# Optimization experiments

Hardware: AMD Instinct MI355X
Metric: run time of the kernel (lower is better)

Reference implementation:

```python
import jax, jax.numpy as jnp
import numpy as np

N = 10000
E = 320000
D = 256


def setup_inputs() -> dict:
    key = jax.random.key(0)
    ks = jax.random.split(key, 10)
    s = 1.0 / np.sqrt(D)
    return {
        "x0": jax.random.normal(ks[0], (N, D), jnp.float32),
        "edge_index": jax.random.randint(ks[1], (2, E), 0, N, jnp.int32),
        "W1": jax.random.normal(ks[2], (D, D), jnp.float32) * s,
        "b1": jax.random.normal(ks[3], (D,), jnp.float32) * s,
        "W2": jax.random.normal(ks[4], (D, D), jnp.float32) * s,
        "b2": jax.random.normal(ks[5], (D,), jnp.float32) * s,
        "wa1": jax.random.normal(ks[6], (D,), jnp.float32) * s,
        "ba1": jax.random.normal(ks[7], (1,), jnp.float32) * s,
        "wa2": jax.random.normal(ks[8], (D,), jnp.float32) * s,
        "ba2": jax.random.normal(ks[9], (1,), jnp.float32) * s,
    }


def reference(x0, edge_index, W1, b1, W2, b2, wa1, ba1, wa2, ba2):
    n = x0.shape[0]
    leaky = lambda v: jax.nn.leaky_relu(v, 0.2)
    x0_i = leaky(x0 @ W1 + b1)                      # [N, D]
    x0_j = leaky(x0 @ W2 + b2)                      # [N, D]
    a1 = x0_i @ wa1 + ba1[0]                        # [N]
    a2 = x0_j @ wa2 + ba2[0]                        # [N]
    row, col = edge_index[0], edge_index[1]
    # sigmoid(a_1 + a_2.T)[row, col] without the dense N x N intermediate
    att = jax.nn.sigmoid(a1[row] + a2[col])         # [E]
    msg = att[:, None] * x0_j[col]                  # [E, D]
    out = jax.ops.segment_sum(msg, row, num_segments=n)  # sparse.mm(attention, x0_j)
    return out + x0
```

## Files before the change

kernel.cpp:

```cpp
#include <hip/hip_runtime.h>
#include <math.h>

#define D 256
#define CAP 128
#define APAD 264

typedef float f32x4 __attribute__((ext_vector_type(4)));
typedef short s16x8 __attribute__((ext_vector_type(8)));
typedef unsigned short u16x8 __attribute__((ext_vector_type(8)));

static __device__ __forceinline__ unsigned short f2bf(float x) {
    union { float f; unsigned u; } v; v.f = x;
    unsigned r = v.u + 0x7fff + ((v.u >> 16) & 1);
    return (unsigned short)(r >> 16);
}
static __device__ __forceinline__ float bf2f(unsigned short h) {
    union { unsigned u; float f; } v; v.u = ((unsigned)h) << 16;
    return v.f;
}

__global__ __launch_bounds__(256) void k_init(
    const float* __restrict__ W1, const float* __restrict__ W2,
    unsigned short* __restrict__ wt, int* __restrict__ curp, int n)
{
    const int i = blockIdx.x * 256 + threadIdx.x;
    if (i < 2 * D * D) {
        int k = i >> 9;
        int j = i & 511;
        float v = (j < D) ? W1[(size_t)k * D + j] : W2[(size_t)k * D + (j - D)];
        wt[(size_t)j * D + k] = f2bf(v);
    }
    if (i < n * 32) curp[i] = 0;
}

__global__ __launch_bounds__(256) void k_mfma_rank(
    const float* __restrict__ x0, const unsigned short* __restrict__ wt,
    const float* __restrict__ b1, const float* __restrict__ b2,
    const float* __restrict__ wa1, const float* __restrict__ wa2,
    const float* __restrict__ ba1, const float* __restrict__ ba2,
    const int* __restrict__ rows, const int* __restrict__ cols,
    int* __restrict__ curp, int* __restrict__ perm,
    unsigned short* __restrict__ x0j, float* __restrict__ a1,
    float* __restrict__ a2, int n, int e, int nrb)
{
    __shared__ unsigned short Atile[32][APAD];
    __shared__ float part[4][32];
    const int t = threadIdx.x;

    if ((int)blockIdx.x < nrb) {
        const int i0 = (blockIdx.x * 256 + t) * 8;
        if (i0 + 7 < e) {
            int4 ra = *(const int4*)&rows[i0];
            int4 rb4 = *(const int4*)&rows[i0 + 4];
            int4 ca = *(const int4*)&cols[i0];
            int4 cb4 = *(const int4*)&cols[i0 + 4];
            int s0 = atomicAdd(&curp[(size_t)ra.x << 5], 1);
            int s1 = atomicAdd(&curp[(size_t)ra.y << 5], 1);
            int s2 = atomicAdd(&curp[(size_t)ra.z << 5], 1);
            int s3 = atomicAdd(&curp[(size_t)ra.w << 5], 1);
            int s4 = atomicAdd(&curp[(size_t)rb4.x << 5], 1);
            int s5 = atomicAdd(&curp[(size_t)rb4.y << 5], 1);
            int s6 = atomicAdd(&curp[(size_t)rb4.z << 5], 1);
            int s7 = atomicAdd(&curp[(size_t)rb4.w << 5], 1);
            if (s0 < CAP) perm[(size_t)ra.x * CAP + s0] = ca.x;
            if (s1 < CAP) perm[(size_t)ra.y * CAP + s1] = ca.y;
            if (s2 < CAP) perm[(size_t)ra.z * CAP + s2] = ca.z;
            if (s3 < CAP) perm[(size_t)ra.w * CAP + s3] = ca.w;
            if (s4 < CAP) perm[(size_t)rb4.x * CAP + s4] = cb4.x;
            if (s5 < CAP) perm[(size_t)rb4.y * CAP + s5] = cb4.y;
            if (s6 < CAP) perm[(size_t)rb4.z * CAP + s6] = cb4.z;
            if (s7 < CAP) perm[(size_t)rb4.w * CAP + s7] = cb4.w;
        } else {
            for (int i = i0; i < e; ++i) {
                int r = rows[i];
                int slot = atomicAdd(&curp[(size_t)r << 5], 1);
                if (slot < CAP) perm[(size_t)r * CAP + slot] = cols[i];
            }
        }
        return;
    }

    const int lane = t & 63, w = t >> 6;
    const int rb = (blockIdx.x - nrb) * 32;
    const int lr = lane & 15;
    const int kg = lane >> 4;

    for (int s = t; s < 32 * 32; s += 256) {
        const int row = s >> 5, seg = s & 31;
        int gr = rb + row; if (gr >= n) gr = n - 1;
        f32x4 v0 = *(const f32x4*)&x0[(size_t)gr * D + seg * 8];
        f32x4 v1 = *(const f32x4*)&x0[(size_t)gr * D + seg * 8 + 4];
        u16x8 o;
        o[0] = f2bf(v0.x); o[1] = f2bf(v0.y); o[2] = f2bf(v0.z); o[3] = f2bf(v0.w);
        o[4] = f2bf(v1.x); o[5] = f2bf(v1.y); o[6] = f2bf(v1.z); o[7] = f2bf(v1.w);
        *(u16x8*)&Atile[row][seg * 8] = o;
    }
    __syncthreads();

    const int cb = w * 128;
    f32x4 acc[2][8] = {};

    #pragma unroll
    for (int ks = 0; ks < 8; ++ks) {
        const int k0 = ks * 32 + kg * 8;
        s16x8 af[2];
        af[0] = *(const s16x8*)&Atile[lr][k0];
        af[1] = *(const s16x8*)&Atile[16 + lr][k0];
        s16x8 bfr[8];
        #pragma unroll
        for (int cf = 0; cf < 8; ++cf)
            bfr[cf] = *(const s16x8*)&wt[(size_t)(cb + cf * 16 + lr) * D + k0];
        #pragma unroll
        for (int rf = 0; rf < 2; ++rf)
            #pragma unroll
            for (int cf = 0; cf < 8; ++cf)
                acc[rf][cf] = __builtin_amdgcn_mfma_f32_16x16x32_bf16(
                    af[rf], bfr[cf], acc[rf][cf], 0, 0, 0);
    }

    const bool isW2 = (w >= 2);
    const float* wav  = isW2 ? wa2 : wa1;
    const float* bias = isW2 ? b2  : b1;
    const int crel = cb - (isW2 ? D : 0);

    float rs[2][4] = {};
    #pragma unroll
    for (int rf = 0; rf < 2; ++rf) {
        #pragma unroll
        for (int cf = 0; cf < 8; ++cf) {
            const int col = crel + cf * 16 + lr;
            const float bv = bias[col], wv = wav[col];
            #pragma unroll
            for (int r = 0; r < 4; ++r) {
                float v = acc[rf][cf][r] + bv;
                v = (v > 0.0f) ? v : 0.2f * v;
                const int row = rb + rf * 16 + kg * 4 + r;
                if (isW2 && row < n) x0j[(size_t)row * D + col] = f2bf(v);
                rs[rf][r] += v * wv;
            }
        }
    }

    #pragma unroll
    for (int rf = 0; rf < 2; ++rf)
        #pragma unroll
        for (int r = 0; r < 4; ++r) {
            float s = rs[rf][r];
            s += __shfl_xor(s, 1, 64);
            s += __shfl_xor(s, 2, 64);
            s += __shfl_xor(s, 4, 64);
            s += __shfl_xor(s, 8, 64);
            if (lr == 0) part[w][rf * 16 + kg * 4 + r] = s;
        }
    __syncthreads();
    if (t < 32) {
        const int row = rb + t;
        if (row < n) {
            a1[row] = part[0][t] + part[1][t] + ba1[0] + ba2[0];
            a2[row] = part[2][t] + part[3][t];
        }
    }
}

__global__ __launch_bounds__(256) void k_agg(
    const unsigned short* __restrict__ x0j, const float* __restrict__ x0,
    const float* __restrict__ a1, const float* __restrict__ a2,
    const int* __restrict__ curp, const int* __restrict__ perm,
    float* __restrict__ out, int n, int nbh)
{
    __shared__ int   scol[4][CAP + 4];
    __shared__ float satt[4][CAP + 4];

    const int w = threadIdx.x >> 6, lane = threadIdx.x & 63;
    const int q = lane >> 4, hl = lane & 15;
    const int phase = blockIdx.x / nbh;
    const int row = (blockIdx.x % nbh) * 4 + w;

    int deg = 0;
    if (row < n) {
        deg = curp[(size_t)row << 5];
        if (deg > CAP) deg = CAP;
        const size_t pbase = (size_t)row * CAP;
        const float a1r = a1[row];

        for (int i = lane; i < deg; i += 64) {
            int c = perm[pbase + i];
            scol[w][i] = c;
            satt[w][i] = 1.0f / (1.0f + __expf(-(a1r + a2[c])));
        }
        if (lane < 4) {
            scol[w][deg + lane] = 0;
            satt[w][deg + lane] = 0.0f;
        }
    }
    __syncthreads();
    if (row >= n) return;

    const int degp = (deg + 3) & ~3;
    const int cbase = phase * 128 + hl * 8;

    float acc[8];
    #pragma unroll
    for (int k = 0; k < 8; ++k) acc[k] = 0.0f;

    for (int j = 0; j < degp; j += 4) {
        const int idx = j + q;
        const float a = satt[w][idx];
        const int   c = scol[w][idx];
        u16x8 v = *(const u16x8*)&x0j[(size_t)c * D + cbase];
        #pragma unroll
        for (int k = 0; k < 8; ++k) acc[k] += a * bf2f(v[k]);
    }

    #pragma unroll
    for (int k = 0; k < 8; ++k) acc[k] += __shfl_xor(acc[k], 16, 64);
    #pragma unroll
    for (int k = 0; k < 8; ++k) acc[k] += __shfl_xor(acc[k], 32, 64);

    float s0, s1;
    if      (q == 0) { s0 = acc[0]; s1 = acc[1]; }
    else if (q == 1) { s0 = acc[2]; s1 = acc[3]; }
    else if (q == 2) { s0 = acc[4]; s1 = acc[5]; }
    else             { s0 = acc[6]; s1 = acc[7]; }

    const int col = cbase + q * 2;
    float2 r = *(const float2*)&x0[(size_t)row * D + col];
    float2 o;
    o.x = r.x + s0; o.y = r.y + s1;
    *(float2*)&out[(size_t)row * D + col] = o;
}

extern "C" void kernel_launch(void* const* d_in, const int* in_sizes, int n_in,
                              void* d_out, int out_size, void* d_ws, size_t ws_size,
                              hipStream_t stream)
{
    const float* x0  = (const float*)d_in[0];
    const int*   ei  = (const int*)d_in[1];
    const float* W1  = (const float*)d_in[2];
    const float* b1  = (const float*)d_in[3];
    const float* W2  = (const float*)d_in[4];
    const float* b2  = (const float*)d_in[5];
    const float* wa1 = (const float*)d_in[6];
    const float* ba1 = (const float*)d_in[7];
    const float* wa2 = (const float*)d_in[8];
    const float* ba2 = (const float*)d_in[9];
    float* out = (float*)d_out;

    const int n = in_sizes[0] / D;
    const int e = in_sizes[1] / 2;
    const int* rows = ei;
    const int* cols = ei + e;

    char* ws = (char*)d_ws;
    unsigned short* wt  = (unsigned short*)ws;
    unsigned short* x0j = wt + (size_t)2 * D * D;
    float* a1   = (float*)(x0j + (size_t)n * D);
    float* a2   = a1 + n;
    int*   curp = (int*)(a2 + n);
    int*   perm = curp + (size_t)n * 32;

    const int ithreads = n * 32;
    k_init<<<(ithreads + 255) / 256, 256, 0, stream>>>(W1, W2, wt, curp, n);
    const int gx = (n + 31) / 32;
    const int nrb = (e / 8 + 255) / 256;
    k_mfma_rank<<<nrb + gx, 256, 0, stream>>>(x0, wt, b1, b2, wa1, wa2,
                                              ba1, ba2, rows, cols, curp, perm,
                                              x0j, a1, a2, n, e, nrb);
    const int nbh = (n + 3) / 4;
    k_agg<<<2 * nbh, 256, 0, stream>>>(x0j, x0, a1, a2, curp, perm, out, n, nbh);
}
```

Measured before the change: 58.14 us.

## Quantize x0_j to per-row int8 and aggregate full rows per wave

Stores the leaky-ReLU x0_j features as uint8 with a per-row absmax scale, computed in the GEMM epilogue, instead of bf16. The scale is packed with a2 and folded into the attention weight, and the zero-point offset is removed with a running sum of weights. The aggregation kernel now has each wave cover all 256 columns of a row with 16-byte loads, instead of two column-half launches. This halves the bytes of the gather, which is bandwidth bound, and removes the duplicate index and attention setup. The cost is a coarser quantization error that may exceed tolerance, plus extra epilogue work and a second block barrier.

```diff
diff --git a/kernel.cpp b/kernel.cpp
--- a/kernel.cpp
+++ b/kernel.cpp
@@ -13,10 +13,6 @@
     union { float f; unsigned u; } v; v.f = x;
     unsigned r = v.u + 0x7fff + ((v.u >> 16) & 1);
     return (unsigned short)(r >> 16);
-}
-static __device__ __forceinline__ float bf2f(unsigned short h) {
-    union { unsigned u; float f; } v; v.u = ((unsigned)h) << 16;
-    return v.f;
 }
 
 __global__ __launch_bounds__(256) void k_init(
@@ -40,11 +36,13 @@
     const float* __restrict__ ba1, const float* __restrict__ ba2,
     const int* __restrict__ rows, const int* __restrict__ cols,
     int* __restrict__ curp, int* __restrict__ perm,
-    unsigned short* __restrict__ x0j, float* __restrict__ a1,
-    float* __restrict__ a2, int n, int e, int nrb)
+    unsigned char* __restrict__ x0j8, float* __restrict__ a1,
+    float2* __restrict__ a2s, int n, int e, int nrb)
 {
     __shared__ unsigned short Atile[32][APAD];
     __shared__ float part[4][32];
+    __shared__ float pmx[2][32];
+    __shared__ float sscale[32];
     const int t = threadIdx.x;
 
     if ((int)blockIdx.x < nrb) {
@@ -123,58 +121,91 @@
     const float* bias = isW2 ? b2  : b1;
     const int crel = cb - (isW2 ? D : 0);
 
+    float bvv[8], wvv[8];
+    #pragma unroll
+    for (int cf = 0; cf < 8; ++cf) {
+        bvv[cf] = bias[crel + cf * 16 + lr];
+        wvv[cf] = wav[crel + cf * 16 + lr];
+    }
+
     float rs[2][4] = {};
-    #pragma unroll
-    for (int rf = 0; rf < 2; ++rf) {
-        #pragma unroll
-        for (int cf = 0; cf < 8; ++cf) {
-            const int col = crel + cf * 16 + lr;
-            const float bv = bias[col], wv = wav[col];
+    float mx[2][4] = {};
+    #pragma unroll
+    for (int rf = 0; rf < 2; ++rf)
+        #pragma unroll
+        for (int cf = 0; cf < 8; ++cf)
             #pragma unroll
             for (int r = 0; r < 4; ++r) {
-                float v = acc[rf][cf][r] + bv;
+                float v = acc[rf][cf][r] + bvv[cf];
                 v = (v > 0.0f) ? v : 0.2f * v;
-                const int row = rb + rf * 16 + kg * 4 + r;
-                if (isW2 && row < n) x0j[(size_t)row * D + col] = f2bf(v);
-                rs[rf][r] += v * wv;
-            }
-        }
-    }
+                rs[rf][r] += v * wvv[cf];
+                mx[rf][r] = fmaxf(mx[rf][r], fabsf(v));
+            }
 
     #pragma unroll
     for (int rf = 0; rf < 2; ++rf)
         #pragma unroll
         for (int r = 0; r < 4; ++r) {
-            float s = rs[rf][r];
-            s += __shfl_xor(s, 1, 64);
-            s += __shfl_xor(s, 2, 64);
-            s += __shfl_xor(s, 4, 64);
-            s += __shfl_xor(s, 8, 64);
-            if (lr == 0) part[w][rf * 16 + kg * 4 + r] = s;
+            float s = rs[rf][r], m = mx[rf][r];
+            #pragma unroll
+            for (int o = 1; o < 16; o <<= 1) {
+                s += __shfl_xor(s, o, 64);
+                m = fmaxf(m, __shfl_xor(m, o, 64));
+            }
+            if (lr == 0) {
+                const int ri = rf * 16 + kg * 4 + r;
+                part[w][ri] = s;
+                if (isW2) pmx[w - 2][ri] = m;
+            }
         }
     __syncthreads();
     if (t < 32) {
         const int row = rb + t;
+        float smax = fmaxf(fmaxf(pmx[0][t], pmx[1][t]), 1e-20f);
+        float sc = smax * (1.0f / 127.0f);
+        sscale[t] = sc;
         if (row < n) {
             a1[row] = part[0][t] + part[1][t] + ba1[0] + ba2[0];
-            a2[row] = part[2][t] + part[3][t];
-        }
+            float2 av; av.x = part[2][t] + part[3][t]; av.y = sc;
+            a2s[row] = av;
+        }
+    }
+    __syncthreads();
+
+    if (isW2) {
+        #pragma unroll
+        for (int rf = 0; rf < 2; ++rf)
+            #pragma unroll
+            for (int r = 0; r < 4; ++r) {
+                const int ri = rf * 16 + kg * 4 + r;
+                const int row = rb + ri;
+                if (row >= n) continue;
+                const float inv_s = 1.0f / sscale[ri];
+                #pragma unroll
+                for (int cf = 0; cf < 8; ++cf) {
+                    const int col = crel + cf * 16 + lr;
+                    float v = acc[rf][cf][r] + bvv[cf];
+                    v = (v > 0.0f) ? v : 0.2f * v;
+                    int qv = (int)rintf(v * inv_s) + 128;
+                    qv = (qv < 0) ? 0 : ((qv > 255) ? 255 : qv);
+                    x0j8[(size_t)row * D + col] = (unsigned char)qv;
+                }
+            }
     }
 }
 
 __global__ __launch_bounds__(256) void k_agg(
-    const unsigned short* __restrict__ x0j, const float* __restrict__ x0,
-    const float* __restrict__ a1, const float* __restrict__ a2,
+    const unsigned char* __restrict__ x0j8, const float* __restrict__ x0,
+    const float* __restrict__ a1, const float2* __restrict__ a2s,
     const int* __restrict__ curp, const int* __restrict__ perm,
-    float* __restrict__ out, int n, int nbh)
+    float* __restrict__ out, int n)
 {
     __shared__ int   scol[4][CAP + 4];
     __shared__ float satt[4][CAP + 4];
 
     const int w = threadIdx.x >> 6, lane = threadIdx.x & 63;
     const int q = lane >> 4, hl = lane & 15;
-    const int phase = blockIdx.x / nbh;
-    const int row = (blockIdx.x % nbh) * 4 + w;
+    const int row = blockIdx.x * 4 + w;
 
     int deg = 0;
     if (row < n) {
@@ -186,7 +217,9 @@
         for (int i = lane; i < deg; i += 64) {
             int c = perm[pbase + i];
             scol[w][i] = c;
-            satt[w][i] = 1.0f / (1.0f + __expf(-(a1r + a2[c])));
+            float2 p = a2s[c];
+            float att = 1.0f / (1.0f + __expf(-(a1r + p.x)));
+            satt[w][i] = att * p.y;
         }
         if (lane < 4) {
             scol[w][deg + lane] = 0;
@@ -197,37 +230,59 @@
     if (row >= n) return;
 
     const int degp = (deg + 3) & ~3;
-    const int cbase = phase * 128 + hl * 8;
-
-    float acc[8];
-    #pragma unroll
-    for (int k = 0; k < 8; ++k) acc[k] = 0.0f;
+
+    float acc[16];
+    #pragma unroll
+    for (int k = 0; k < 16; ++k) acc[k] = 0.0f;
+    float corr = 0.0f;
 
     for (int j = 0; j < degp; j += 4) {
         const int idx = j + q;
-        const float a = satt[w][idx];
-        const int   c = scol[w][idx];
-        u16x8 v = *(const u16x8*)&x0j[(size_t)c * D + cbase];
-        #pragma unroll
-        for (int k = 0; k < 8; ++k) acc[k] += a * bf2f(v[k]);
-    }
-
-    #pragma unroll
-    for (int k = 0; k < 8; ++k) acc[k] += __shfl_xor(acc[k], 16, 64);
-    #pragma unroll
-    for (int k = 0; k < 8; ++k) acc[k] += __shfl_xor(acc[k], 32, 64);
-
-    float s0, s1;
-    if      (q == 0) { s0 = acc[0]; s1 = acc[1]; }
-    else if (q == 1) { s0 = acc[2]; s1 = acc[3]; }
-    else if (q == 2) { s0 = acc[4]; s1 = acc[5]; }
-    else             { s0 = acc[6]; s1 = acc[7]; }
-
-    const int col = cbase + q * 2;
-    float2 r = *(const float2*)&x0[(size_t)row * D + col];
-    float2 o;
-    o.x = r.x + s0; o.y = r.y + s1;
-    *(float2*)&out[(size_t)row * D + col] = o;
+        const float as = satt[w][idx];
+        const int   c  = scol[w][idx];
+        uint4 v = *(const uint4*)&x0j8[(size_t)c * D + hl * 16];
+        corr += as;
+        acc[0]  += as * (float)( v.x        & 255);
+        acc[1]  += as * (float)((v.x >>  8) & 255);
+        acc[2]  += as * (float)((v.x >> 16) & 255);
+        acc[3]  += as * (float)( v.x >> 24);
+        acc[4]  += as * (float)( v.y        & 255);
+        acc[5]  += as * (float)((v.y >>  8) & 255);
+        acc[6]  += as * (float)((v.y >> 16) & 255);
+        acc[7]  += as * (float)( v.y >> 24);
+        acc[8]  += as * (float)( v.z        & 255);
+        acc[9]  += as * (float)((v.z >>  8) & 255);
+        acc[10] += as * (float)((v.z >> 16) & 255);
+        acc[11] += as * (float)( v.z >> 24);
+        acc[12] += as * (float)( v.w        & 255);
+        acc[13] += as * (float)((v.w >>  8) & 255);
+        acc[14] += as * (float)((v.w >> 16) & 255);
+        acc[15] += as * (float)( v.w >> 24);
+    }
+
+    #pragma unroll
+    for (int k = 0; k < 16; ++k) acc[k] += __shfl_xor(acc[k], 16, 64);
+    corr += __shfl_xor(corr, 16, 64);
+    #pragma unroll
+    for (int k = 0; k < 16; ++k) acc[k] += __shfl_xor(acc[k], 32, 64);
+    corr += __shfl_xor(corr, 32, 64);
+
+    const float bias128 = 128.0f * corr;
+
+    float s0, s1, s2, s3;
+    if      (q == 0) { s0 = acc[0];  s1 = acc[1];  s2 = acc[2];  s3 = acc[3];  }
+    else if (q == 1) { s0 = acc[4];  s1 = acc[5];  s2 = acc[6];  s3 = acc[7];  }
+    else if (q == 2) { s0 = acc[8];  s1 = acc[9];  s2 = acc[10]; s3 = acc[11]; }
+    else             { s0 = acc[12]; s1 = acc[13]; s2 = acc[14]; s3 = acc[15]; }
+
+    const int col = hl * 16 + q * 4;
+    f32x4 r = *(const f32x4*)&x0[(size_t)row * D + col];
+    f32x4 o;
+    o.x = r.x + s0 - bias128;
+    o.y = r.y + s1 - bias128;
+    o.z = r.z + s2 - bias128;
+    o.w = r.w + s3 - bias128;
+    *(f32x4*)&out[(size_t)row * D + col] = o;
 }
 
 extern "C" void kernel_launch(void* const* d_in, const int* in_sizes, int n_in,
@@ -252,12 +307,12 @@
     const int* cols = ei + e;
 
     char* ws = (char*)d_ws;
-    unsigned short* wt  = (unsigned short*)ws;
-    unsigned short* x0j = wt + (size_t)2 * D * D;
-    float* a1   = (float*)(x0j + (size_t)n * D);
-    float* a2   = a1 + n;
-    int*   curp = (int*)(a2 + n);
-    int*   perm = curp + (size_t)n * 32;
+    unsigned short* wt   = (unsigned short*)ws;
+    unsigned char*  x0j8 = (unsigned char*)(wt + (size_t)2 * D * D);
+    float*  a1   = (float*)(x0j8 + (size_t)n * D);
+    float2* a2s  = (float2*)(a1 + n);
+    int*    curp = (int*)(a2s + n);
+    int*    perm = curp + (size_t)n * 32;
 
     const int ithreads = n * 32;
     k_init<<<(ithreads + 255) / 256, 256, 0, stream>>>(W1, W2, wt, curp, n);
@@ -265,7 +320,6 @@
     const int nrb = (e / 8 + 255) / 256;
     k_mfma_rank<<<nrb + gx, 256, 0, stream>>>(x0, wt, b1, b2, wa1, wa2,
                                               ba1, ba2, rows, cols, curp, perm,
-                                              x0j, a1, a2, n, e, nrb);
-    const int nbh = (n + 3) / 4;
-    k_agg<<<2 * nbh, 256, 0, stream>>>(x0j, x0, a1, a2, curp, perm, out, n, nbh);
-}
+                                              x0j8, a1, a2s, n, e, nrb);
+    k_agg<<<(n + 3) / 4, 256, 0, stream>>>(x0j8, x0, a1, a2s, curp, perm, out, n);
+}
```

Result: faster. 53.80 us (-7.5%).
